# Performance work log

Measured on AMD Instinct MI355X. Metric: run time of the kernel, lower is better.

The kernel has to match this reference:

```python
import jax, jax.numpy as jnp
import numpy as np

NEG_SLOPE = 0.2  # PyG GATConv default leaky_relu slope
EPS = 1e-16


def setup_inputs() -> dict:
    key = jax.random.key(0)
    ks = jax.random.split(key, 8)
    N, E, F = 50000, 1600000, 128
    L, H, C = 3, 4, 32  # layers, heads, per-head channels; H*C == F
    Dh = 32             # MLP hidden (== hidden_channels)
    x = jax.random.normal(ks[0], (N, F), jnp.float32)
    edge_index = jax.random.randint(ks[1], (2, E), 0, N, jnp.int32)
    W = jax.random.normal(ks[2], (L, F, H * C), jnp.float32) * 0.1
    att_src = jax.random.normal(ks[3], (L, H, C), jnp.float32) * 0.1
    att_dst = jax.random.normal(ks[4], (L, H, C), jnp.float32) * 0.1
    b_conv = jnp.zeros((L, H * C), jnp.float32)
    W1 = jax.random.normal(ks[5], (F + H * C, Dh), jnp.float32) * 0.1
    b1 = jnp.zeros((Dh,), jnp.float32)
    W2 = jax.random.normal(ks[6], (Dh, 1), jnp.float32) * 0.1
    b2 = jnp.zeros((1,), jnp.float32)
    return {"x": x, "edge_index": edge_index, "W": W, "att_src": att_src,
            "att_dst": att_dst, "b_conv": b_conv, "W1": W1, "b1": b1,
            "W2": W2, "b2": b2}


def _gat_layer(x, src, dst, W, a_s, a_d, b, N):
    H, C = a_s.shape
    h = (x @ W).reshape(N, H, C)                      # [N,H,C]
    alpha_s = jnp.sum(h * a_s, axis=-1)               # [N,H]
    alpha_d = jnp.sum(h * a_d, axis=-1)               # [N,H]
    e = jax.nn.leaky_relu(alpha_s[src] + alpha_d[dst], NEG_SLOPE)  # [E,H]
    # segment softmax over incoming edges of each dst node
    m = jax.ops.segment_max(e, dst, num_segments=N)
    ex = jnp.exp(e - m[dst])
    s = jax.ops.segment_sum(ex, dst, num_segments=N)
    a = ex / (s[dst] + EPS)                           # [E,H]
    out = jax.ops.segment_sum(h[src] * a[:, :, None], dst, num_segments=N)
    return out.reshape(N, H * C) + b


def reference(x, edge_index, W, att_src, att_dst, b_conv, W1, b1, W2, b2):
    N = x.shape[0]
    loops = jnp.arange(N, dtype=edge_index.dtype)
    src = jnp.concatenate([edge_index[0], loops])  # PyG GATConv adds self loops
    dst = jnp.concatenate([edge_index[1], loops])
    x0 = x
    for l in range(W.shape[0]):
        x = _gat_layer(x, src, dst, W[l], att_src[l], att_dst[l], b_conv[l], N)
    h = jnp.concatenate([x, x0], axis=-1)
    h = jax.nn.relu(h @ W1 + b1)
    return jax.nn.sigmoid(h @ W2 + b2)
```

## Files before the change

### kernel.cpp

```cpp
#include <hip/hip_runtime.h>

#define NEG_SLOPE 0.2f
#define EPSF 1e-16f
#define SEG_SHIFT 12

typedef unsigned int uint;
typedef unsigned short ushort;
typedef __attribute__((ext_vector_type(8))) short short8;
typedef __attribute__((ext_vector_type(4))) float floatx4;
typedef __attribute__((ext_vector_type(4))) uint uintx4;

static __device__ __forceinline__ ushort f2bf(float f) {
    uint u = __float_as_uint(f);
    return (ushort)((u + 0x7FFFu + ((u >> 16) & 1u)) >> 16);
}
static __device__ __forceinline__ uint pack2(float a, float b) {
    return (uint)f2bf(a) | ((uint)f2bf(b) << 16);
}
static __device__ __forceinline__ float bf_lo(uint p) { return __uint_as_float(p << 16); }
static __device__ __forceinline__ float bf_hi(uint p) { return __uint_as_float(p & 0xFFFF0000u); }
static __device__ __forceinline__ short8 u2s8(uint4 v) {
    union { uint4 u; short8 s; } c; c.u = v; return c.s;
}
static __device__ __forceinline__ void load_lds16(const void* g, void* l) {
    __builtin_amdgcn_global_load_lds(
        (const __attribute__((address_space(1))) void*)g,
        (__attribute__((address_space(3))) void*)l, 16, 0, 0);
}

__global__ __launch_bounds__(256) void prep_count_kernel(
    const float* __restrict__ W, const float* __restrict__ W1,
    const float* __restrict__ x, uint4* __restrict__ Wp,
    uint4* __restrict__ W1p, uint4* __restrict__ xb,
    const int* __restrict__ ei, int E, int NB,
    int* __restrict__ bucket_count, int L, int N, int nbPrep)
{
    __shared__ int cnt[256];
    if ((int)blockIdx.x >= nbPrep) {
        cnt[threadIdx.x] = 0;
        __syncthreads();
        const int base = (blockIdx.x - nbPrep) * 2048 + threadIdx.x;
#pragma unroll
        for (int j = 0; j < 8; ++j) {
            int idx = base + j * 256;
            if (idx < E) atomicAdd(&cnt[ei[E + idx] >> 8], 1);
        }
        __syncthreads();
        int c = cnt[threadIdx.x];
        if ((int)threadIdx.x < NB && c) atomicAdd(&bucket_count[threadIdx.x], c);
        return;
    }
    int id = blockIdx.x * 256 + threadIdx.x;
    const int nW = L * 2048;
    const int nX = N * 16;
    if (id < nW) {
        int l = id >> 11, s = id & 2047;
        int chunk = s >> 7, col = s & 127;
        const float* wp = W + (size_t)l * 16384 + (chunk * 8) * 128 + col;
        uint4 pk;
        pk.x = pack2(wp[0],   wp[128]);
        pk.y = pack2(wp[256], wp[384]);
        pk.z = pack2(wp[512], wp[640]);
        pk.w = pack2(wp[768], wp[896]);
        Wp[id] = pk;
    } else if (id < nW + 1024) {
        int s = id - nW;
        int chunk = s >> 5, col = s & 31;
        const float* wp = W1 + (chunk * 8) * 32 + col;
        uint4 pk;
        pk.x = pack2(wp[0],   wp[32]);
        pk.y = pack2(wp[64],  wp[96]);
        pk.z = pack2(wp[128], wp[160]);
        pk.w = pack2(wp[192], wp[224]);
        W1p[s] = pk;
    } else if (id < nW + 1024 + nX) {
        int xid = id - nW - 1024;
        int row = xid >> 4, c8 = xid & 15;
        const float4* xp = (const float4*)(x + (size_t)row * 128 + c8 * 8);
        float4 v0 = xp[0], v1 = xp[1];
        uint4 pk;
        pk.x = pack2(v0.x, v0.y); pk.y = pack2(v0.z, v0.w);
        pk.z = pack2(v1.x, v1.y); pk.w = pack2(v1.z, v1.w);
        xb[xid] = pk;
    }
}

__global__ __launch_bounds__(256) void gemm_alpha_kernel(
    const uint4* __restrict__ xb, const uint4* __restrict__ Wp,
    const float* __restrict__ att_s, const float* __restrict__ att_d,
    uint* __restrict__ h2, float* __restrict__ alpha_s,
    float* __restrict__ alpha_d, int N)
{
    __shared__ __align__(16) uint4 sW[2048];
    __shared__ __align__(16) uint4 sX[16 * 65];

    const int t = threadIdx.x;
    const int wb = t & ~63;
    const int rowBase = blockIdx.x * 64;

#pragma unroll
    for (int i = 0; i < 8; ++i)
        load_lds16(Wp + i * 256 + t, sW + i * 256 + wb);

#pragma unroll
    for (int i = 0; i < 4; ++i) {
        int f = t + i * 256;
        int row = f >> 4, c8 = f & 15;
        uint4 v = make_uint4(0u, 0u, 0u, 0u);
        if (rowBase + row < N) v = xb[(size_t)(rowBase + row) * 16 + c8];
        sX[c8 * 65 + row] = v;
    }
    __syncthreads();

    const int w = t >> 6, lane = t & 63, q = lane >> 4, l15 = lane & 15;
    short8 xf[4];
#pragma unroll
    for (int s = 0; s < 4; ++s)
        xf[s] = u2s8(sX[(4 * s + q) * 65 + 16 * w + l15]);

    floatx4 acc[8];
#pragma unroll
    for (int ct = 0; ct < 8; ++ct) acc[ct] = (floatx4){0.f, 0.f, 0.f, 0.f};
#pragma unroll
    for (int ct = 0; ct < 8; ++ct) {
#pragma unroll
        for (int s = 0; s < 4; ++s) {
            short8 wf = u2s8(sW[(4 * s + q) * 128 + 16 * ct + l15]);
            acc[ct] = __builtin_amdgcn_mfma_f32_16x16x32_bf16(wf, xf[s], acc[ct], 0, 0, 0);
        }
    }

    const int node = rowBase + 16 * w + l15;
    if (node < N) {
        uint2* hp = (uint2*)(h2 + (size_t)node * 64);
#pragma unroll
        for (int ct = 0; ct < 8; ++ct) {
            uint2 o;
            o.x = pack2(acc[ct][0], acc[ct][1]);
            o.y = pack2(acc[ct][2], acc[ct][3]);
            hp[(8 * ct + 2 * q) >> 1] = o;
        }
    }
    float ps[4], pd[4];
#pragma unroll
    for (int hd = 0; hd < 4; ++hd) {
        const float4 as0 = *(const float4*)(att_s + 32 * hd + 4 * q);
        const float4 as1 = *(const float4*)(att_s + 32 * hd + 16 + 4 * q);
        const float4 ad0 = *(const float4*)(att_d + 32 * hd + 4 * q);
        const float4 ad1 = *(const float4*)(att_d + 32 * hd + 16 + 4 * q);
        floatx4 c0 = acc[2 * hd], c1 = acc[2 * hd + 1];
        ps[hd] = c0[0] * as0.x + c0[1] * as0.y + c0[2] * as0.z + c0[3] * as0.w
               + c1[0] * as1.x + c1[1] * as1.y + c1[2] * as1.z + c1[3] * as1.w;
        pd[hd] = c0[0] * ad0.x + c0[1] * ad0.y + c0[2] * ad0.z + c0[3] * ad0.w
               + c1[0] * ad1.x + c1[1] * ad1.y + c1[2] * ad1.z + c1[3] * ad1.w;
    }
#pragma unroll
    for (int hd = 0; hd < 4; ++hd) {
        ps[hd] += __shfl_xor(ps[hd], 16);
        ps[hd] += __shfl_xor(ps[hd], 32);
        pd[hd] += __shfl_xor(pd[hd], 16);
        pd[hd] += __shfl_xor(pd[hd], 32);
    }
    if (node < N) {
        alpha_s[(size_t)node * 4 + q] = ps[q];
        alpha_d[(size_t)node * 4 + q] = pd[q];
    }
}

__global__ __launch_bounds__(256) void bucket_scan_kernel(
    const int* __restrict__ bucket_count, int NB,
    int* __restrict__ bucket_base, int* __restrict__ bucket_cursor,
    int* __restrict__ row_start, int N)
{
    __shared__ int s[256];
    const int t = threadIdx.x;
    int v = (t < NB) ? bucket_count[t] : 0;
    s[t] = v;
    __syncthreads();
    for (int off = 1; off < 256; off <<= 1) {
        int x = s[t];
        int a = (t >= off) ? s[t - off] : 0;
        __syncthreads();
        s[t] = x + a;
        __syncthreads();
    }
    int ex = s[t] - v;
    if (t < NB) { bucket_base[t] = ex; bucket_cursor[t] = ex; }
    if (t == 255) { bucket_base[NB] = s[255]; row_start[N] = s[255]; }
}

__global__ __launch_bounds__(256) void distribute_kernel(
    const int* __restrict__ ei, int E, int NB,
    int* __restrict__ bucket_cursor, uint* __restrict__ bdata)
{
    __shared__ int cnt[256];
    __shared__ int bbase[256];
    cnt[threadIdx.x] = 0;
    __syncthreads();
    const int base = blockIdx.x * 4096 + threadIdx.x;
    int srcs[16], dsts[16], rank[16];
#pragma unroll
    for (int j = 0; j < 16; ++j) {
        int idx = base + j * 256;
        if (idx < E) {
            srcs[j] = ei[idx];
            dsts[j] = ei[E + idx];
            rank[j] = atomicAdd(&cnt[dsts[j] >> 8], 1);
        } else dsts[j] = -1;
    }
    __syncthreads();
    {
        int c = cnt[threadIdx.x];
        bbase[threadIdx.x] = ((int)threadIdx.x < NB && c) ? atomicAdd(&bucket_cursor[threadIdx.x], c) : 0;
    }
    __syncthreads();
#pragma unroll
    for (int j = 0; j < 16; ++j) {
        if (dsts[j] >= 0) {
            int b = dsts[j] >> 8;
            bdata[bbase[b] + rank[j]] = (uint)srcs[j] | ((uint)(dsts[j] & 255) << 16);
        }
    }
}

#define BCAP 12800
__global__ __launch_bounds__(256) void bucket_csr_kernel(
    const uint* __restrict__ bdata, const int* __restrict__ bucket_base,
    int* __restrict__ row_start, ushort* __restrict__ csr_src, int N)
{
    __shared__ int hist[4096];
    __shared__ int cur[4096];
    __shared__ int scn[256];
    __shared__ ushort buf[BCAP];
    const int b = blockIdx.x;
    const int t = threadIdx.x;
    const int beg = bucket_base[b];
    const int sz = bucket_base[b + 1] - beg;
#pragma unroll
    for (int j = 0; j < 16; ++j) hist[t * 16 + j] = 0;
    __syncthreads();
    for (int i = t; i < sz; i += 256) {
        uint d = bdata[beg + i];
        int key = (int)((d >> 16) << 4) | (int)((d & 0xFFFFu) >> SEG_SHIFT);
        atomicAdd(&hist[key], 1);
    }
    __syncthreads();
    int local[16]; int s = 0;
#pragma unroll
    for (int j = 0; j < 16; ++j) { local[j] = hist[t * 16 + j]; s += local[j]; }
    scn[t] = s;
    __syncthreads();
    for (int off = 1; off < 256; off <<= 1) {
        int x = scn[t];
        int a = (t >= off) ? scn[t - off] : 0;
        __syncthreads();
        scn[t] = x + a;
        __syncthreads();
    }
    int run = scn[t] - s;
#pragma unroll
    for (int j = 0; j < 16; ++j) { cur[t * 16 + j] = run; run += local[j]; }
    __syncthreads();
    int node = b * 256 + t;
    if (node < N) row_start[node] = beg + cur[t << 4];
    __syncthreads();
    if (sz <= BCAP) {
        for (int i = t; i < sz; i += 256) {
            uint d = bdata[beg + i];
            int key = (int)((d >> 16) << 4) | (int)((d & 0xFFFFu) >> SEG_SHIFT);
            int pos = atomicAdd(&cur[key], 1);
            buf[pos] = (ushort)(d & 0xFFFFu);
        }
        __syncthreads();
        for (int i = t; i < sz; i += 256) csr_src[beg + i] = buf[i];
    } else {
        for (int i = t; i < sz; i += 256) {
            uint d = bdata[beg + i];
            int key = (int)((d >> 16) << 4) | (int)((d & 0xFFFFu) >> SEG_SHIFT);
            int pos = atomicAdd(&cur[key], 1);
            csr_src[beg + pos] = (ushort)(d & 0xFFFFu);
        }
    }
}

__global__ __launch_bounds__(256) void agg_csr_kernel(
    const ushort* __restrict__ csr_src, const int* __restrict__ row_start,
    const float* __restrict__ alpha_s, const float* __restrict__ alpha_d,
    const uint* __restrict__ h2, const float* __restrict__ b,
    uint* __restrict__ outb, int N)
{
    const int g = (blockIdx.x * 256 + threadIdx.x) >> 4;
    const int l = threadIdx.x & 15;
    if (g >= N) return;
    const int head = l >> 2;
    const char* hbase = (const char*)h2 + (size_t)l * 16;

    const float ad = alpha_d[g * 4 + head];

    float e = alpha_s[g * 4 + head] + ad;
    e = e > 0.f ? e : NEG_SLOPE * e;
    float ex = __expf(e);
    uint4 q = *(const uint4*)(hbase + (uint)g * 256u);
    float a0 = ex * bf_lo(q.x), a1 = ex * bf_hi(q.x);
    float a2 = ex * bf_lo(q.y), a3 = ex * bf_hi(q.y);
    float a4 = ex * bf_lo(q.z), a5 = ex * bf_hi(q.z);
    float a6 = ex * bf_lo(q.w), a7 = ex * bf_hi(q.w);
    float sx = ex;

    const int beg = row_start[g];
    const int end = row_start[g + 1];
    int k = beg;
    for (; k + 4 <= end; k += 4) {
        uint s0 = csr_src[k], s1 = csr_src[k + 1];
        uint s2 = csr_src[k + 2], s3 = csr_src[k + 3];
        uint4 q0 = *(const uint4*)(hbase + s0 * 256u);
        uint4 q1 = *(const uint4*)(hbase + s1 * 256u);
        uint4 q2 = *(const uint4*)(hbase + s2 * 256u);
        uint4 q3 = *(const uint4*)(hbase + s3 * 256u);
        float e0 = alpha_s[s0 * 4 + head] + ad;
        float e1 = alpha_s[s1 * 4 + head] + ad;
        float e2 = alpha_s[s2 * 4 + head] + ad;
        float e3 = alpha_s[s3 * 4 + head] + ad;
        e0 = e0 > 0.f ? e0 : NEG_SLOPE * e0;
        e1 = e1 > 0.f ? e1 : NEG_SLOPE * e1;
        e2 = e2 > 0.f ? e2 : NEG_SLOPE * e2;
        e3 = e3 > 0.f ? e3 : NEG_SLOPE * e3;
        float x0 = __expf(e0), x1 = __expf(e1);
        float x2 = __expf(e2), x3 = __expf(e3);
        a0 += x0 * bf_lo(q0.x) + x1 * bf_lo(q1.x) + x2 * bf_lo(q2.x) + x3 * bf_lo(q3.x);
        a1 += x0 * bf_hi(q0.x) + x1 * bf_hi(q1.x) + x2 * bf_hi(q2.x) + x3 * bf_hi(q3.x);
        a2 += x0 * bf_lo(q0.y) + x1 * bf_lo(q1.y) + x2 * bf_lo(q2.y) + x3 * bf_lo(q3.y);
        a3 += x0 * bf_hi(q0.y) + x1 * bf_hi(q1.y) + x2 * bf_hi(q2.y) + x3 * bf_hi(q3.y);
        a4 += x0 * bf_lo(q0.z) + x1 * bf_lo(q1.z) + x2 * bf_lo(q2.z) + x3 * bf_lo(q3.z);
        a5 += x0 * bf_hi(q0.z) + x1 * bf_hi(q1.z) + x2 * bf_hi(q2.z) + x3 * bf_hi(q3.z);
        a6 += x0 * bf_lo(q0.w) + x1 * bf_lo(q1.w) + x2 * bf_lo(q2.w) + x3 * bf_lo(q3.w);
        a7 += x0 * bf_hi(q0.w) + x1 * bf_hi(q1.w) + x2 * bf_hi(q2.w) + x3 * bf_hi(q3.w);
        sx += x0 + x1 + x2 + x3;
    }
    for (; k < end; ++k) {
        uint s0 = csr_src[k];
        float e0 = alpha_s[s0 * 4 + head] + ad;
        uint4 q0 = *(const uint4*)(hbase + s0 * 256u);
        e0 = e0 > 0.f ? e0 : NEG_SLOPE * e0;
        float x0 = __expf(e0);
        a0 += x0 * bf_lo(q0.x); a1 += x0 * bf_hi(q0.x);
        a2 += x0 * bf_lo(q0.y); a3 += x0 * bf_hi(q0.y);
        a4 += x0 * bf_lo(q0.z); a5 += x0 * bf_hi(q0.z);
        a6 += x0 * bf_lo(q0.w); a7 += x0 * bf_hi(q0.w);
        sx += x0;
    }
    const float inv = 1.f / (sx + EPSF);
    const float4 b0 = ((const float4*)b)[l * 2];
    const float4 b1 = ((const float4*)b)[l * 2 + 1];
    uintx4 o;
    o.x = pack2(b0.x + a0 * inv, b0.y + a1 * inv);
    o.y = pack2(b0.z + a2 * inv, b0.w + a3 * inv);
    o.z = pack2(b1.x + a4 * inv, b1.y + a5 * inv);
    o.w = pack2(b1.z + a6 * inv, b1.w + a7 * inv);
    __builtin_nontemporal_store(o, (uintx4*)(outb + (size_t)g * 64 + l * 4));
}

__global__ __launch_bounds__(256) void mlp_kernel(
    const uint4* __restrict__ xb3, const uint4* __restrict__ xb0,
    const uint4* __restrict__ W1p, const float* __restrict__ b1,
    const float* __restrict__ W2, const float* __restrict__ b2,
    float* __restrict__ out, int N)
{
    __shared__ __align__(16) uint4 sA[32 * 65];
    __shared__ __align__(16) uint4 sB[32 * 32];
    const int t = threadIdx.x;
    const int wb = t & ~63;
    const int rowBase = blockIdx.x * 64;

#pragma unroll
    for (int i = 0; i < 4; ++i)
        load_lds16(W1p + i * 256 + t, sB + i * 256 + wb);
#pragma unroll
    for (int i = 0; i < 8; ++i) {
        int f = t + i * 256;
        int c = f & 31, row = f >> 5;
        uint4 v = make_uint4(0u, 0u, 0u, 0u);
        int grow = rowBase + row;
        if (grow < N)
            v = (c < 16) ? xb3[(size_t)grow * 16 + c]
                         : xb0[(size_t)grow * 16 + (c - 16)];
        sA[c * 65 + row] = v;
    }
    __syncthreads();

    const int w = t >> 6, lane = t & 63, q = lane >> 4, l15 = lane & 15;
    floatx4 acc0 = (floatx4){0.f, 0.f, 0.f, 0.f};
    floatx4 acc1 = (floatx4){0.f, 0.f, 0.f, 0.f};
#pragma unroll
    for (int s = 0; s < 8; ++s) {
        short8 a = u2s8(sA[(4 * s + q) * 65 + 16 * w + l15]);
        acc0 = __builtin_amdgcn_mfma_f32_16x16x32_bf16(a, u2s8(sB[(4 * s + q) * 32 + l15]), acc0, 0, 0, 0);
        acc1 = __builtin_amdgcn_mfma_f32_16x16x32_bf16(a, u2s8(sB[(4 * s + q) * 32 + 16 + l15]), acc1, 0, 0, 0);
    }
    const float b1a = b1[l15], b1b = b1[16 + l15];
    const float w2a = W2[l15], w2b = W2[16 + l15];
    const float b2v = b2[0];
#pragma unroll
    for (int r = 0; r < 4; ++r) {
        int row = rowBase + 16 * w + 4 * q + r;
        float v0 = acc0[r] + b1a; v0 = v0 > 0.f ? v0 : 0.f;
        float v1 = acc1[r] + b1b; v1 = v1 > 0.f ? v1 : 0.f;
        float p = v0 * w2a + v1 * w2b;
        p += __shfl_xor(p, 1);
        p += __shfl_xor(p, 2);
        p += __shfl_xor(p, 4);
        p += __shfl_xor(p, 8);
        if (l15 == 0 && row < N)
            out[row] = 1.f / (1.f + __expf(-(p + b2v)));
    }
}

extern "C" void kernel_launch(void* const* d_in, const int* in_sizes, int n_in,
                              void* d_out, int out_size, void* d_ws, size_t ws_size,
                              hipStream_t stream)
{
    const float* x       = (const float*)d_in[0];
    const int*   ei      = (const int*)d_in[1];
    const float* W       = (const float*)d_in[2];
    const float* att_src = (const float*)d_in[3];
    const float* att_dst = (const float*)d_in[4];
    const float* b_conv  = (const float*)d_in[5];
    const float* W1      = (const float*)d_in[6];
    const float* b1      = (const float*)d_in[7];
    const float* W2      = (const float*)d_in[8];
    const float* b2      = (const float*)d_in[9];
    float* outp = (float*)d_out;

    const int N = in_sizes[0] / 128;
    const int E = in_sizes[1] / 2;
    const int L = in_sizes[2] / (128 * 128);
    const int NB = (N + 255) >> 8;

    char* ws = (char*)d_ws;
    uint*  h2      = (uint*)ws;
    uint4* xb0     = (uint4*)(h2 + (size_t)N * 64);
    uint4* xb      = xb0 + (size_t)N * 16;
    float* alpha_s = (float*)(xb + (size_t)N * 16);
    float* alpha_d = alpha_s + (size_t)N * 4;
    uint4* Wp      = (uint4*)(alpha_d + (size_t)N * 4);
    uint4* W1p     = Wp + (size_t)L * 2048;
    int* bucket_count  = (int*)(W1p + 1024);
    int* bucket_base   = bucket_count + 256;
    int* bucket_cursor = bucket_base + 260;
    int* row_start     = bucket_cursor + 256;
    uint* bdata        = (uint*)(row_start + N + 1);
    ushort* csr_src    = (ushort*)(bdata + E);

    const int nbEc = (E + 2047) / 2048;
    const int nbEd = (E + 4095) / 4096;
    const int prepItems = L * 2048 + 1024 + N * 16;
    const int nbPrep = (prepItems + 255) / 256;

    (void)hipMemsetAsync(bucket_count, 0, 256 * sizeof(int), stream);

    prep_count_kernel<<<nbPrep + nbEc, 256, 0, stream>>>(
        W, W1, x, Wp, W1p, xb0, ei, E, NB, bucket_count, L, N, nbPrep);

    bucket_scan_kernel<<<1, 256, 0, stream>>>(bucket_count, NB, bucket_base,
                                              bucket_cursor, row_start, N);
    distribute_kernel<<<nbEd, 256, 0, stream>>>(ei, E, NB, bucket_cursor, bdata);
    bucket_csr_kernel<<<NB, 256, 0, stream>>>(bdata, bucket_base, row_start,
                                              csr_src, N);

    for (int l = 0; l < L; ++l) {
        const uint4* xin = (l == 0) ? xb0 : xb;
        const uint4* Wl  = Wp + (size_t)l * 2048;
        const float* asl = att_src + (size_t)l * 128;
        const float* adl = att_dst + (size_t)l * 128;
        const float* bl  = b_conv + (size_t)l * 128;

        gemm_alpha_kernel<<<(N + 63) / 64, 256, 0, stream>>>(
            xin, Wl, asl, adl, h2, alpha_s, alpha_d, N);

        agg_csr_kernel<<<(N * 16 + 255) / 256, 256, 0, stream>>>(
            csr_src, row_start, alpha_s, alpha_d, h2, bl, (uint*)xb, N);
    }

    mlp_kernel<<<(N + 63) / 64, 256, 0, stream>>>(
        xb, xb0, W1p, b1, W2, b2, outp, N);
}
```

Measured before the change: 368.9 us.

## Fuse edge distribution with first-layer GEMM and fold bucket scan into consumers

Removes the single-block bucket scan kernel. Each distribute block and each CSR block now recomputes the 256-entry prefix scan from bucket_count itself. The distribute step and the layer-0 GEMM/alpha computation are merged into one launch, with the block index selecting the role, so the independent work overlaps and there are fewer launches. The CSR sub-bucket key granularity is halved (SEG_SHIFT 13, 8 sub-bins per node), which cuts LDS histogram size and init work but gives coarser source ordering within each row. The price is redundant scans in every block and a larger shared-memory footprint for the distribute blocks.

```diff
diff --git a/kernel.cpp b/kernel.cpp
--- a/kernel.cpp
+++ b/kernel.cpp
@@ -2,7 +2,7 @@
 
 #define NEG_SLOPE 0.2f
 #define EPSF 1e-16f
-#define SEG_SHIFT 12
+#define SEG_SHIFT 13
 
 typedef unsigned int uint;
 typedef unsigned short ushort;
@@ -26,6 +26,89 @@
     __builtin_amdgcn_global_load_lds(
         (const __attribute__((address_space(1))) void*)g,
         (__attribute__((address_space(3))) void*)l, 16, 0, 0);
+}
+
+#define GA_LDS_BYTES (2048 * 16 + 16 * 65 * 16)
+
+static __device__ __forceinline__ void gemm_body(
+    char* smraw, const uint4* __restrict__ xb, const uint4* __restrict__ Wp,
+    const float* __restrict__ att_s, const float* __restrict__ att_d,
+    uint* __restrict__ h2, float* __restrict__ alpha_s,
+    float* __restrict__ alpha_d, int N, int rowBase)
+{
+    uint4* sW = (uint4*)smraw;
+    uint4* sX = sW + 2048;
+
+    const int t = threadIdx.x;
+    const int wb = t & ~63;
+
+#pragma unroll
+    for (int i = 0; i < 8; ++i)
+        load_lds16(Wp + i * 256 + t, sW + i * 256 + wb);
+
+#pragma unroll
+    for (int i = 0; i < 4; ++i) {
+        int f = t + i * 256;
+        int row = f >> 4, c8 = f & 15;
+        uint4 v = make_uint4(0u, 0u, 0u, 0u);
+        if (rowBase + row < N) v = xb[(size_t)(rowBase + row) * 16 + c8];
+        sX[c8 * 65 + row] = v;
+    }
+    __syncthreads();
+
+    const int w = t >> 6, lane = t & 63, q = lane >> 4, l15 = lane & 15;
+    short8 xf[4];
+#pragma unroll
+    for (int s = 0; s < 4; ++s)
+        xf[s] = u2s8(sX[(4 * s + q) * 65 + 16 * w + l15]);
+
+    floatx4 acc[8];
+#pragma unroll
+    for (int ct = 0; ct < 8; ++ct) acc[ct] = (floatx4){0.f, 0.f, 0.f, 0.f};
+#pragma unroll
+    for (int ct = 0; ct < 8; ++ct) {
+#pragma unroll
+        for (int s = 0; s < 4; ++s) {
+            short8 wf = u2s8(sW[(4 * s + q) * 128 + 16 * ct + l15]);
+            acc[ct] = __builtin_amdgcn_mfma_f32_16x16x32_bf16(wf, xf[s], acc[ct], 0, 0, 0);
+        }
+    }
+
+    const int node = rowBase + 16 * w + l15;
+    if (node < N) {
+        uint2* hp = (uint2*)(h2 + (size_t)node * 64);
+#pragma unroll
+        for (int ct = 0; ct < 8; ++ct) {
+            uint2 o;
+            o.x = pack2(acc[ct][0], acc[ct][1]);
+            o.y = pack2(acc[ct][2], acc[ct][3]);
+            hp[4 * ct + q] = o;
+        }
+    }
+    float ps[4], pd[4];
+#pragma unroll
+    for (int hd = 0; hd < 4; ++hd) {
+        const float4 as0 = *(const float4*)(att_s + 32 * hd + 4 * q);
+        const float4 as1 = *(const float4*)(att_s + 32 * hd + 16 + 4 * q);
+        const float4 ad0 = *(const float4*)(att_d + 32 * hd + 4 * q);
+        const float4 ad1 = *(const float4*)(att_d + 32 * hd + 16 + 4 * q);
+        floatx4 c0 = acc[2 * hd], c1 = acc[2 * hd + 1];
+        ps[hd] = c0[0] * as0.x + c0[1] * as0.y + c0[2] * as0.z + c0[3] * as0.w
+               + c1[0] * as1.x + c1[1] * as1.y + c1[2] * as1.z + c1[3] * as1.w;
+        pd[hd] = c0[0] * ad0.x + c0[1] * ad0.y + c0[2] * ad0.z + c0[3] * ad0.w
+               + c1[0] * ad1.x + c1[1] * ad1.y + c1[2] * ad1.z + c1[3] * ad1.w;
+    }
+#pragma unroll
+    for (int hd = 0; hd < 4; ++hd) {
+        ps[hd] += __shfl_xor(ps[hd], 16);
+        ps[hd] += __shfl_xor(ps[hd], 32);
+        pd[hd] += __shfl_xor(pd[hd], 16);
+        pd[hd] += __shfl_xor(pd[hd], 32);
+    }
+    if (node < N) {
+        alpha_s[(size_t)node * 4 + q] = ps[q];
+        alpha_d[(size_t)node * 4 + q] = pd[q];
+    }
 }
 
 __global__ __launch_bounds__(256) void prep_count_kernel(
@@ -85,119 +168,28 @@
     }
 }
 
-__global__ __launch_bounds__(256) void gemm_alpha_kernel(
+__global__ __launch_bounds__(256) void dist_gemm_kernel(
+    const int* __restrict__ ei, int E, int NB,
+    const int* __restrict__ bucket_count, int* __restrict__ bucket_cursor,
+    uint* __restrict__ bdata, int nbEd,
     const uint4* __restrict__ xb, const uint4* __restrict__ Wp,
     const float* __restrict__ att_s, const float* __restrict__ att_d,
     uint* __restrict__ h2, float* __restrict__ alpha_s,
     float* __restrict__ alpha_d, int N)
 {
-    __shared__ __align__(16) uint4 sW[2048];
-    __shared__ __align__(16) uint4 sX[16 * 65];
-
+    __shared__ __align__(16) char smraw[GA_LDS_BYTES];
     const int t = threadIdx.x;
-    const int wb = t & ~63;
-    const int rowBase = blockIdx.x * 64;
-
-#pragma unroll
-    for (int i = 0; i < 8; ++i)
-        load_lds16(Wp + i * 256 + t, sW + i * 256 + wb);
-
-#pragma unroll
-    for (int i = 0; i < 4; ++i) {
-        int f = t + i * 256;
-        int row = f >> 4, c8 = f & 15;
-        uint4 v = make_uint4(0u, 0u, 0u, 0u);
-        if (rowBase + row < N) v = xb[(size_t)(rowBase + row) * 16 + c8];
-        sX[c8 * 65 + row] = v;
-    }
-    __syncthreads();
-
-    const int w = t >> 6, lane = t & 63, q = lane >> 4, l15 = lane & 15;
-    short8 xf[4];
-#pragma unroll
-    for (int s = 0; s < 4; ++s)
-        xf[s] = u2s8(sX[(4 * s + q) * 65 + 16 * w + l15]);
-
-    floatx4 acc[8];
-#pragma unroll
-    for (int ct = 0; ct < 8; ++ct) acc[ct] = (floatx4){0.f, 0.f, 0.f, 0.f};
-#pragma unroll
-    for (int ct = 0; ct < 8; ++ct) {
-#pragma unroll
-        for (int s = 0; s < 4; ++s) {
-            short8 wf = u2s8(sW[(4 * s + q) * 128 + 16 * ct + l15]);
-            acc[ct] = __builtin_amdgcn_mfma_f32_16x16x32_bf16(wf, xf[s], acc[ct], 0, 0, 0);
-        }
-    }
-
-    const int node = rowBase + 16 * w + l15;
-    if (node < N) {
-        uint2* hp = (uint2*)(h2 + (size_t)node * 64);
-#pragma unroll
-        for (int ct = 0; ct < 8; ++ct) {
-            uint2 o;
-            o.x = pack2(acc[ct][0], acc[ct][1]);
-            o.y = pack2(acc[ct][2], acc[ct][3]);
-            hp[(8 * ct + 2 * q) >> 1] = o;
-        }
-    }
-    float ps[4], pd[4];
-#pragma unroll
-    for (int hd = 0; hd < 4; ++hd) {
-        const float4 as0 = *(const float4*)(att_s + 32 * hd + 4 * q);
-        const float4 as1 = *(const float4*)(att_s + 32 * hd + 16 + 4 * q);
-        const float4 ad0 = *(const float4*)(att_d + 32 * hd + 4 * q);
-        const float4 ad1 = *(const float4*)(att_d + 32 * hd + 16 + 4 * q);
-        floatx4 c0 = acc[2 * hd], c1 = acc[2 * hd + 1];
-        ps[hd] = c0[0] * as0.x + c0[1] * as0.y + c0[2] * as0.z + c0[3] * as0.w
-               + c1[0] * as1.x + c1[1] * as1.y + c1[2] * as1.z + c1[3] * as1.w;
-        pd[hd] = c0[0] * ad0.x + c0[1] * ad0.y + c0[2] * ad0.z + c0[3] * ad0.w
-               + c1[0] * ad1.x + c1[1] * ad1.y + c1[2] * ad1.z + c1[3] * ad1.w;
-    }
-#pragma unroll
-    for (int hd = 0; hd < 4; ++hd) {
-        ps[hd] += __shfl_xor(ps[hd], 16);
-        ps[hd] += __shfl_xor(ps[hd], 32);
-        pd[hd] += __shfl_xor(pd[hd], 16);
-        pd[hd] += __shfl_xor(pd[hd], 32);
-    }
-    if (node < N) {
-        alpha_s[(size_t)node * 4 + q] = ps[q];
-        alpha_d[(size_t)node * 4 + q] = pd[q];
-    }
-}
-
-__global__ __launch_bounds__(256) void bucket_scan_kernel(
-    const int* __restrict__ bucket_count, int NB,
-    int* __restrict__ bucket_base, int* __restrict__ bucket_cursor,
-    int* __restrict__ row_start, int N)
-{
-    __shared__ int s[256];
-    const int t = threadIdx.x;
-    int v = (t < NB) ? bucket_count[t] : 0;
-    s[t] = v;
-    __syncthreads();
-    for (int off = 1; off < 256; off <<= 1) {
-        int x = s[t];
-        int a = (t >= off) ? s[t - off] : 0;
-        __syncthreads();
-        s[t] = x + a;
-        __syncthreads();
-    }
-    int ex = s[t] - v;
-    if (t < NB) { bucket_base[t] = ex; bucket_cursor[t] = ex; }
-    if (t == 255) { bucket_base[NB] = s[255]; row_start[N] = s[255]; }
-}
-
-__global__ __launch_bounds__(256) void distribute_kernel(
-    const int* __restrict__ ei, int E, int NB,
-    int* __restrict__ bucket_cursor, uint* __restrict__ bdata)
-{
-    __shared__ int cnt[256];
-    __shared__ int bbase[256];
-    cnt[threadIdx.x] = 0;
-    __syncthreads();
-    const int base = blockIdx.x * 4096 + threadIdx.x;
+    if ((int)blockIdx.x >= nbEd) {
+        gemm_body(smraw, xb, Wp, att_s, att_d, h2, alpha_s, alpha_d, N,
+                  (blockIdx.x - nbEd) * 64);
+        return;
+    }
+    int* cnt = (int*)smraw;
+    int* sc  = cnt + 256;
+    int* bb  = sc + 256;
+    cnt[t] = 0;
+    __syncthreads();
+    const int base = blockIdx.x * 4096 + t;
     int srcs[16], dsts[16], rank[16];
 #pragma unroll
     for (int j = 0; j < 16; ++j) {
@@ -209,45 +201,80 @@
         } else dsts[j] = -1;
     }
     __syncthreads();
-    {
-        int c = cnt[threadIdx.x];
-        bbase[threadIdx.x] = ((int)threadIdx.x < NB && c) ? atomicAdd(&bucket_cursor[threadIdx.x], c) : 0;
-    }
+    int bc = (t < NB) ? bucket_count[t] : 0;
+    sc[t] = bc;
+    __syncthreads();
+    for (int off = 1; off < 256; off <<= 1) {
+        int x = sc[t];
+        int a = (t >= off) ? sc[t - off] : 0;
+        __syncthreads();
+        sc[t] = x + a;
+        __syncthreads();
+    }
+    int gbase = sc[t] - bc;
+    int c = cnt[t];
+    bb[t] = (t < NB && c) ? (gbase + atomicAdd(&bucket_cursor[t], c)) : 0;
     __syncthreads();
 #pragma unroll
     for (int j = 0; j < 16; ++j) {
         if (dsts[j] >= 0) {
             int b = dsts[j] >> 8;
-            bdata[bbase[b] + rank[j]] = (uint)srcs[j] | ((uint)(dsts[j] & 255) << 16);
-        }
-    }
+            bdata[bb[b] + rank[j]] = (uint)srcs[j] | ((uint)(dsts[j] & 255) << 16);
+        }
+    }
+}
+
+__global__ __launch_bounds__(256) void gemm_alpha_kernel(
+    const uint4* __restrict__ xb, const uint4* __restrict__ Wp,
+    const float* __restrict__ att_s, const float* __restrict__ att_d,
+    uint* __restrict__ h2, float* __restrict__ alpha_s,
+    float* __restrict__ alpha_d, int N)
+{
+    __shared__ __align__(16) char smraw[GA_LDS_BYTES];
+    gemm_body(smraw, xb, Wp, att_s, att_d, h2, alpha_s, alpha_d, N,
+              blockIdx.x * 64);
 }
 
 #define BCAP 12800
 __global__ __launch_bounds__(256) void bucket_csr_kernel(
-    const uint* __restrict__ bdata, const int* __restrict__ bucket_base,
-    int* __restrict__ row_start, ushort* __restrict__ csr_src, int N)
-{
-    __shared__ int hist[4096];
-    __shared__ int cur[4096];
+    const uint* __restrict__ bdata, const int* __restrict__ bucket_count,
+    int NB, int E, int* __restrict__ row_start, ushort* __restrict__ csr_src,
+    int N)
+{
+    __shared__ int hist[2048];
+    __shared__ int cur[2048];
     __shared__ int scn[256];
+    __shared__ int sb[256];
     __shared__ ushort buf[BCAP];
     const int b = blockIdx.x;
     const int t = threadIdx.x;
-    const int beg = bucket_base[b];
-    const int sz = bucket_base[b + 1] - beg;
-#pragma unroll
-    for (int j = 0; j < 16; ++j) hist[t * 16 + j] = 0;
+
+    int bc = (t < NB) ? bucket_count[t] : 0;
+    sb[t] = bc;
+    __syncthreads();
+    for (int off = 1; off < 256; off <<= 1) {
+        int x = sb[t];
+        int a = (t >= off) ? sb[t - off] : 0;
+        __syncthreads();
+        sb[t] = x + a;
+        __syncthreads();
+    }
+    const int beg = (b > 0) ? sb[b - 1] : 0;
+    const int sz = sb[b] - beg;
+    if (b == 0 && t == 0) row_start[N] = E;
+
+#pragma unroll
+    for (int j = 0; j < 8; ++j) hist[t * 8 + j] = 0;
     __syncthreads();
     for (int i = t; i < sz; i += 256) {
         uint d = bdata[beg + i];
-        int key = (int)((d >> 16) << 4) | (int)((d & 0xFFFFu) >> SEG_SHIFT);
+        int key = (int)((d >> 16) << 3) | (int)((d & 0xFFFFu) >> SEG_SHIFT);
         atomicAdd(&hist[key], 1);
     }
     __syncthreads();
-    int local[16]; int s = 0;
-#pragma unroll
-    for (int j = 0; j < 16; ++j) { local[j] = hist[t * 16 + j]; s += local[j]; }
+    int local[8]; int s = 0;
+#pragma unroll
+    for (int j = 0; j < 8; ++j) { local[j] = hist[t * 8 + j]; s += local[j]; }
     scn[t] = s;
     __syncthreads();
     for (int off = 1; off < 256; off <<= 1) {
@@ -259,15 +286,15 @@
     }
     int run = scn[t] - s;
 #pragma unroll
-    for (int j = 0; j < 16; ++j) { cur[t * 16 + j] = run; run += local[j]; }
+    for (int j = 0; j < 8; ++j) { cur[t * 8 + j] = run; run += local[j]; }
     __syncthreads();
     int node = b * 256 + t;
-    if (node < N) row_start[node] = beg + cur[t << 4];
+    if (node < N) row_start[node] = beg + cur[t << 3];
     __syncthreads();
     if (sz <= BCAP) {
         for (int i = t; i < sz; i += 256) {
             uint d = bdata[beg + i];
-            int key = (int)((d >> 16) << 4) | (int)((d & 0xFFFFu) >> SEG_SHIFT);
+            int key = (int)((d >> 16) << 3) | (int)((d & 0xFFFFu) >> SEG_SHIFT);
             int pos = atomicAdd(&cur[key], 1);
             buf[pos] = (ushort)(d & 0xFFFFu);
         }
@@ -276,7 +303,7 @@
     } else {
         for (int i = t; i < sz; i += 256) {
             uint d = bdata[beg + i];
-            int key = (int)((d >> 16) << 4) | (int)((d & 0xFFFFu) >> SEG_SHIFT);
+            int key = (int)((d >> 16) << 3) | (int)((d & 0xFFFFu) >> SEG_SHIFT);
             int pos = atomicAdd(&cur[key], 1);
             csr_src[beg + pos] = (ushort)(d & 0xFFFFu);
         }
@@ -445,42 +472,40 @@
     uint4* Wp      = (uint4*)(alpha_d + (size_t)N * 4);
     uint4* W1p     = Wp + (size_t)L * 2048;
     int* bucket_count  = (int*)(W1p + 1024);
-    int* bucket_base   = bucket_count + 256;
-    int* bucket_cursor = bucket_base + 260;
+    int* bucket_cursor = bucket_count + 256;
     int* row_start     = bucket_cursor + 256;
     uint* bdata        = (uint*)(row_start + N + 1);
     ushort* csr_src    = (ushort*)(bdata + E);
 
     const int nbEc = (E + 2047) / 2048;
     const int nbEd = (E + 4095) / 4096;
+    const int gBlocks = (N + 63) / 64;
     const int prepItems = L * 2048 + 1024 + N * 16;
     const int nbPrep = (prepItems + 255) / 256;
 
-    (void)hipMemsetAsync(bucket_count, 0, 256 * sizeof(int), stream);
+    (void)hipMemsetAsync(bucket_count, 0, 512 * sizeof(int), stream);
 
     prep_count_kernel<<<nbPrep + nbEc, 256, 0, stream>>>(
         W, W1, x, Wp, W1p, xb0, ei, E, NB, bucket_count, L, N, nbPrep);
 
-    bucket_scan_kernel<<<1, 256, 0, stream>>>(bucket_count, NB, bucket_base,
-                                              bucket_cursor, row_start, N);
-    distribute_kernel<<<nbEd, 256, 0, stream>>>(ei, E, NB, bucket_cursor, bdata);
-    bucket_csr_kernel<<<NB, 256, 0, stream>>>(bdata, bucket_base, row_start,
-                                              csr_src, N);
+    dist_gemm_kernel<<<nbEd + gBlocks, 256, 0, stream>>>(
+        ei, E, NB, bucket_count, bucket_cursor, bdata, nbEd,
+        xb0, Wp, att_src, att_dst, h2, alpha_s, alpha_d, N);
+
+    bucket_csr_kernel<<<NB, 256, 0, stream>>>(bdata, bucket_count, NB, E,
+                                              row_start, csr_src, N);
 
     for (int l = 0; l < L; ++l) {
-        const uint4* xin = (l == 0) ? xb0 : xb;
-        const uint4* Wl  = Wp + (size_t)l * 2048;
-        const float* asl = att_src + (size_t)l * 128;
-        const float* adl = att_dst + (size_t)l * 128;
-        const float* bl  = b_conv + (size_t)l * 128;
-
-        gemm_alpha_kernel<<<(N + 63) / 64, 256, 0, stream>>>(
-            xin, Wl, asl, adl, h2, alpha_s, alpha_d, N);
-
+        if (l > 0) {
+            gemm_alpha_kernel<<<gBlocks, 256, 0, stream>>>(
+                xb, Wp + (size_t)l * 2048, att_src + (size_t)l * 128,
+                att_dst + (size_t)l * 128, h2, alpha_s, alpha_d, N);
+        }
         agg_csr_kernel<<<(N * 16 + 255) / 256, 256, 0, stream>>>(
-            csr_src, row_start, alpha_s, alpha_d, h2, bl, (uint*)xb, N);
-    }
-
-    mlp_kernel<<<(N + 63) / 64, 256, 0, stream>>>(
+            csr_src, row_start, alpha_s, alpha_d, h2,
+            b_conv + (size_t)l * 128, (uint*)xb, N);
+    }
+
+    mlp_kernel<<<gBlocks, 256, 0, stream>>>(
         xb, xb0, W1p, b1, W2, b2, outp, N);
 }
```

New measurement: 354.7 us. -3.9%, faster.
